# Kernel optimization log

Measured on AMD Instinct MI355X. Metric: run time of the kernel, lower is better.

Reference implementation:

```python
import jax, jax.numpy as jnp
import numpy as np

# DeepSeek-V2 MLA dims (one tensor-parallel shard of 8)
H = 5120          # hidden size
S = 2048          # seq len
B = 1
NH = 16           # 128 heads / 8 devices
Q_LORA = 1536
KV_LORA = 512
NOPE = 128
ROPE = 64
QK = NOPE + ROPE  # 192 per-head q/k dim
VD = 128          # v head dim
DEVICE_NUM = 8
EPS = 1e-6


def rms_norm(x, w):
    v = jnp.mean(jnp.square(x.astype(jnp.float32)), axis=-1, keepdims=True)
    return (x * jax.lax.rsqrt(v + EPS)).astype(x.dtype) * w


def rope_cos_sin(position_ids, dim=ROPE, base=10000.0):
    inv_freq = 1.0 / (base ** (jnp.arange(0, dim, 2, dtype=jnp.float32) / dim))
    freqs = position_ids.astype(jnp.float32)[..., None] * inv_freq       # [B,S,dim/2]
    emb = jnp.concatenate([freqs, freqs], axis=-1)                        # [B,S,dim]
    return jnp.cos(emb), jnp.sin(emb)


def apply_rope(x, cos, sin):
    # DeepSeek interleaved reorder: view(b,h,s,d//2,2).transpose(-1,-2).reshape
    b, h, s, d = x.shape
    x = x.reshape(b, h, s, d // 2, 2).transpose(0, 1, 2, 4, 3).reshape(b, h, s, d)
    x1, x2 = x[..., : d // 2], x[..., d // 2:]
    rot = jnp.concatenate([-x2, x1], axis=-1)
    return x * cos[:, None] + rot * sin[:, None]


def setup_inputs() -> dict:
    key = jax.random.key(0)
    ks = jax.random.split(key, 8)
    sc = 0.02
    hidden_states = jax.random.normal(ks[0], (B, S, H), dtype=jnp.float32)
    position_ids = jnp.arange(S, dtype=jnp.int64 if jax.config.jax_enable_x64 else jnp.int32)[None, :].repeat(B, 0)
    attention_mask = jnp.triu(jnp.full((S, S), -1e9, dtype=jnp.float32), 1)[None, None]
    return {
        "hidden_states": hidden_states,
        "position_ids": position_ids,
        "attention_mask": attention_mask,
        "ln_w": jnp.ones((H,), jnp.float32),
        "q_a_w": jax.random.normal(ks[1], (Q_LORA, H), jnp.float32) * sc,
        "q_a_ln_w": jnp.ones((Q_LORA,), jnp.float32),
        "q_b_w": jax.random.normal(ks[2], (NH * QK, Q_LORA), jnp.float32) * sc,
        "kv_a_w": jax.random.normal(ks[3], (KV_LORA + ROPE, H), jnp.float32) * sc,
        "kv_a_ln_w": jnp.ones((KV_LORA,), jnp.float32),
        "kv_b_w": jax.random.normal(ks[4], (NH * (NOPE + VD), KV_LORA), jnp.float32) * sc,
        "o_w": jax.random.normal(ks[5], (H, NH * VD), jnp.float32) * sc,
    }


def reference(hidden_states, position_ids, attention_mask, ln_w, q_a_w, q_a_ln_w,
              q_b_w, kv_a_w, kv_a_ln_w, kv_b_w, o_w):
    b, s, _ = hidden_states.shape
    residual = hidden_states * (1.0 / DEVICE_NUM)
    x = rms_norm(hidden_states, ln_w)

    # Q path: low-rank down-proj + RMSNorm + up-proj
    q = rms_norm(x @ q_a_w.T, q_a_ln_w) @ q_b_w.T                # [b,s,NH*QK]
    q = q.reshape(b, s, NH, QK).transpose(0, 2, 1, 3)            # [b,NH,s,QK]
    q_nope, q_pe = q[..., :NOPE], q[..., NOPE:]

    # KV path: compressed latent + shared rope key
    ckv = x @ kv_a_w.T                                           # [b,s,KV_LORA+ROPE]
    c_kv, k_pe = ckv[..., :KV_LORA], ckv[..., KV_LORA:]
    k_pe = k_pe.reshape(b, s, 1, ROPE).transpose(0, 2, 1, 3)     # [b,1,s,ROPE]
    kv = rms_norm(c_kv, kv_a_ln_w) @ kv_b_w.T                    # [b,s,NH*(NOPE+VD)]
    kv = kv.reshape(b, s, NH, NOPE + VD).transpose(0, 2, 1, 3)
    k_nope, v = kv[..., :NOPE], kv[..., NOPE:]

    cos, sin = rope_cos_sin(position_ids)
    q_pe = apply_rope(q_pe, cos, sin)
    k_pe = apply_rope(k_pe, cos, sin)

    k = jnp.concatenate([k_nope, jnp.broadcast_to(k_pe, (b, NH, s, ROPE))], axis=-1)
    qf = jnp.concatenate([q_nope, q_pe], axis=-1)

    scores = jnp.einsum('bhqd,bhkd->bhqk', qf, k) * (1.0 / np.sqrt(QK))
    scores = scores + attention_mask
    probs = jax.nn.softmax(scores, axis=-1)
    attn = jnp.einsum('bhqk,bhkd->bhqd', probs, v)               # [b,NH,s,VD]

    out = attn.transpose(0, 2, 1, 3).reshape(b, s, NH * VD) @ o_w.T
    hidden = residual + out
    return hidden.astype(jnp.float32), k.astype(jnp.float32), v.astype(jnp.float32)
```

## Files before the change

### kernel.cpp

```cpp
#include <hip/hip_runtime.h>
#include <math.h>

typedef unsigned short u16;
typedef unsigned int u32;
typedef __attribute__((ext_vector_type(8))) short short8;
typedef __attribute__((ext_vector_type(4))) float f32x4;

#define NHEADS 16
static const int S      = 2048;
static const int Hd     = 5120;
static const int QLORA  = 1536;
static const int KVLORA = 512;
static const int NQK    = 192;
static const int NVD    = 128;
static const int QDIM   = 3072;
static const int KVDIM  = 4096;
static const int NFUSE  = 2176;

__device__ __forceinline__ u16 f2bf(float f) {
    union { float f; u32 u; } v; v.f = f;
    u32 r = v.u + 0x7FFFu + ((v.u >> 16) & 1u);
    return (u16)(r >> 16);
}
__device__ __forceinline__ float bf2f(u16 h) {
    union { u32 u; float f; } v; v.u = (u32)h << 16; return v.f;
}

__global__ void convert_bf16_kernel(const float* __restrict__ src, u16* __restrict__ dst,
                                    int n_src, int n_total) {
    int i = (blockIdx.x * 256 + threadIdx.x) * 4;
    if (i >= n_total) return;
    union { u16 h[4]; uint2 u; } p;
    if (i < n_src) {
        float4 v = *(const float4*)(src + i);
        p.h[0] = f2bf(v.x); p.h[1] = f2bf(v.y); p.h[2] = f2bf(v.z); p.h[3] = f2bf(v.w);
    } else {
        p.h[0] = p.h[1] = p.h[2] = p.h[3] = 0;
    }
    *(uint2*)(dst + i) = p.u;
}

__global__ void rmsnorm_bf16_kernel(const float* in, const float* __restrict__ w,
                                    u16* out, int D, int in_stride, int out_stride) {
    int row = blockIdx.x;
    const float* x = in + (size_t)row * in_stride;
    u16* y = out + (size_t)row * out_stride;
    float ss = 0.f;
    for (int i = threadIdx.x; i < D; i += blockDim.x) { float v = x[i]; ss += v * v; }
    #pragma unroll
    for (int off = 32; off > 0; off >>= 1) ss += __shfl_xor(ss, off);
    __shared__ float wsum[8];
    int wid = threadIdx.x >> 6, lane = threadIdx.x & 63;
    if (lane == 0) wsum[wid] = ss;
    __syncthreads();
    float tot = 0.f;
    int nw = blockDim.x >> 6;
    for (int i = 0; i < nw; ++i) tot += wsum[i];
    float scale = rsqrtf(tot / (float)D + 1e-6f);
    for (int i = threadIdx.x; i < D; i += blockDim.x) y[i] = f2bf(x[i] * scale * w[i]);
}

__global__ void rmsnorm_bf16in_kernel(const u16* in, const float* __restrict__ w,
                                      u16* out, int D, int in_stride, int out_stride) {
    int row = blockIdx.x;
    const u16* x = in + (size_t)row * in_stride;
    u16* y = out + (size_t)row * out_stride;
    float ss = 0.f;
    for (int i = threadIdx.x; i < D; i += blockDim.x) { float v = bf2f(x[i]); ss += v * v; }
    #pragma unroll
    for (int off = 32; off > 0; off >>= 1) ss += __shfl_xor(ss, off);
    __shared__ float wsum[8];
    int wid = threadIdx.x >> 6, lane = threadIdx.x & 63;
    if (lane == 0) wsum[wid] = ss;
    __syncthreads();
    float tot = 0.f;
    int nw = blockDim.x >> 6;
    for (int i = 0; i < nw; ++i) tot += wsum[i];
    float scale = rsqrtf(tot / (float)D + 1e-6f);
    for (int i = threadIdx.x; i < D; i += blockDim.x) y[i] = f2bf(bf2f(x[i]) * scale * w[i]);
}

template<int BM, bool SWZ, bool OBF>
__global__ __launch_bounds__(256) void gemm_k(
    const u16* __restrict__ A, const u16* __restrict__ B, void* __restrict__ Cv,
    int M, int N, int K, const float* __restrict__ resid) {
    constexpr int MR = BM / 32;
    __shared__ u16 As[4][BM * 32];
    __shared__ u16 Bs[4][128 * 32];

    int bm, bn;
    if constexpr (SWZ) {
        const int lin = blockIdx.x + blockIdx.y * gridDim.x;
        const int nwg = gridDim.x * gridDim.y;
        const int xcd = lin & 7, off = lin >> 3;
        const int q = nwg >> 3, r = nwg & 7;
        const int wg = (xcd < r ? xcd * (q + 1) : r * (q + 1) + (xcd - r) * q) + off;
        bm = (wg % gridDim.y) * BM;
        bn = (wg / gridDim.y) * 128;
    } else {
        bm = blockIdx.y * BM;
        bn = blockIdx.x * 128;
    }

    const int tid = threadIdx.x;
    const int w = tid >> 6, lane = tid & 63;
    const int wr = w >> 1, wc = w & 1;
    const int fr = lane & 15, kg = lane >> 4;

    f32x4 acc[MR][4];
    #pragma unroll
    for (int i = 0; i < MR; ++i)
        #pragma unroll
        for (int j = 0; j < 4; ++j) acc[i][j] = (f32x4){0.f, 0.f, 0.f, 0.f};

    const int srow = lane >> 2;
    const int scol = (lane & 3) * 8;
    const u16* Ap0 = A + (size_t)(bm + w * (BM / 4) + srow) * K + scol;
    const u16* Ap1 = Ap0 + (size_t)16 * K;
    const u16* Bp0 = B + (size_t)(bn + w * 32 + srow) * K + scol;
    const u16* Bp1 = Bp0 + (size_t)16 * K;
    const int lda0 = (w * (BM / 4)) * 32;
    const int lda1 = (w * (BM / 4) + 16) * 32;
    const int ldb0 = (w * 32) * 32;
    const int ldb1 = (w * 32 + 16) * 32;

    auto STAGE = [&](int buf, int kk) {
        __builtin_amdgcn_global_load_lds(
            (const __attribute__((address_space(1))) void*)(Ap0 + kk),
            (__attribute__((address_space(3))) void*)&As[buf][lda0], 16, 0, 0);
        if constexpr (BM == 128)
            __builtin_amdgcn_global_load_lds(
                (const __attribute__((address_space(1))) void*)(Ap1 + kk),
                (__attribute__((address_space(3))) void*)&As[buf][lda1], 16, 0, 0);
        __builtin_amdgcn_global_load_lds(
            (const __attribute__((address_space(1))) void*)(Bp0 + kk),
            (__attribute__((address_space(3))) void*)&Bs[buf][ldb0], 16, 0, 0);
        __builtin_amdgcn_global_load_lds(
            (const __attribute__((address_space(1))) void*)(Bp1 + kk),
            (__attribute__((address_space(3))) void*)&Bs[buf][ldb1], 16, 0, 0);
    };
    auto COMP = [&](int buf) {
        short8 af[MR], bfr[4];
        #pragma unroll
        for (int i = 0; i < MR; ++i)
            af[i] = *(const short8*)&As[buf][(wr * (BM / 2) + i * 16 + fr) * 32 + kg * 8];
        #pragma unroll
        for (int i = 0; i < 4; ++i)
            bfr[i] = *(const short8*)&Bs[buf][(wc * 64 + i * 16 + fr) * 32 + kg * 8];
        #pragma unroll
        for (int mi = 0; mi < MR; ++mi)
            #pragma unroll
            for (int ni = 0; ni < 4; ++ni)
                acc[mi][ni] = __builtin_amdgcn_mfma_f32_16x16x32_bf16(af[mi], bfr[ni],
                                                                      acc[mi][ni], 0, 0, 0);
    };

    const int nk = K >> 5;
    STAGE(0, 0);
    STAGE(1, 32);
    for (int kt = 0; kt < nk; ++kt) {
        if (kt + 2 < nk) {
            STAGE((kt + 2) & 3, (kt + 2) << 5);
            if constexpr (BM == 128) asm volatile("s_waitcnt vmcnt(8)" ::: "memory");
            else                     asm volatile("s_waitcnt vmcnt(6)" ::: "memory");
        } else if (kt + 1 < nk) {
            if constexpr (BM == 128) asm volatile("s_waitcnt vmcnt(4)" ::: "memory");
            else                     asm volatile("s_waitcnt vmcnt(3)" ::: "memory");
        } else {
            asm volatile("s_waitcnt vmcnt(0)" ::: "memory");
        }
        __builtin_amdgcn_s_barrier();
        COMP(kt & 3);
    }

    #pragma unroll
    for (int mi = 0; mi < MR; ++mi)
        #pragma unroll
        for (int ni = 0; ni < 4; ++ni)
            #pragma unroll
            for (int r2 = 0; r2 < 4; ++r2) {
                int row = bm + wr * (BM / 2) + mi * 16 + kg * 4 + r2;
                int col = bn + wc * 64 + ni * 16 + fr;
                size_t idx = (size_t)row * N + col;
                float v = acc[mi][ni][r2];
                if constexpr (OBF) {
                    ((u16*)Cv)[idx] = f2bf(v);
                } else {
                    if (resid) v += resid[idx] * 0.125f;
                    ((float*)Cv)[idx] = v;
                }
            }
}

__global__ void prep_q_kernel(const u16* __restrict__ Qb, const int* __restrict__ pos,
                              u16* __restrict__ Qbf) {
    const int s = blockIdx.x;
    const int t = threadIdx.x;
    const u16* qrow = Qb + (size_t)s * QDIM;
    {
        int i = t * 4;
        int hh = i >> 7, d = i & 127;
        uint2 v = *(const uint2*)(qrow + hh * NQK + d);
        *(uint2*)(Qbf + ((size_t)hh * S + s) * NQK + d) = v;
    }
    {
        int hh = t >> 5, j = t & 31;
        float ps = (float)pos[s];
        float inv_freq = 1.0f / powf(10000.0f, (float)j * (1.0f / 32.0f));
        float ang = ps * inv_freq;
        float c = cosf(ang), sn = sinf(ang);
        const u16* pe = qrow + hh * NQK + 128;
        float a = bf2f(pe[2 * j]), b = bf2f(pe[2 * j + 1]);
        u16* dst = Qbf + ((size_t)hh * S + s) * NQK;
        dst[128 + j] = f2bf(a * c - b * sn);
        dst[160 + j] = f2bf(b * c + a * sn);
    }
}

__global__ __launch_bounds__(256) void build_kv64_kernel(
    const u16* __restrict__ KVb, const u16* __restrict__ CF,
    const int* __restrict__ pos_ids,
    float* __restrict__ Kout, float* __restrict__ Vout,
    u16* __restrict__ Kbf, u16* __restrict__ Vtb) {
    const int s0 = blockIdx.x * 64;
    const int h  = blockIdx.y;
    const int t  = threadIdx.x;
    __shared__ u16 T[64][132];

    #pragma unroll
    for (int it = 0; it < 4; ++it) {
        int i = t + it * 256;
        int row = i >> 4, c8 = (i & 15) * 8;
        int s = s0 + row;
        union { uint4 u; u16 hx[8]; } v;
        v.u = *(const uint4*)(KVb + (size_t)s * KVDIM + h * 256 + c8);
        size_t kidx = ((size_t)h * S + s) * NQK + c8;
        *(uint4*)(Kbf + kidx) = v.u;
        float4 f0 = {bf2f(v.hx[0]), bf2f(v.hx[1]), bf2f(v.hx[2]), bf2f(v.hx[3])};
        float4 f1 = {bf2f(v.hx[4]), bf2f(v.hx[5]), bf2f(v.hx[6]), bf2f(v.hx[7])};
        *(float4*)(Kout + kidx) = f0;
        *(float4*)(Kout + kidx + 4) = f1;
    }
    #pragma unroll
    for (int it = 0; it < 4; ++it) {
        int i = t + it * 256;
        int row = i >> 4, c8 = (i & 15) * 8;
        int s = s0 + row;
        union { uint4 u; uint2 d[2]; u16 hx[8]; } v;
        v.u = *(const uint4*)(KVb + (size_t)s * KVDIM + h * 256 + 128 + c8);
        *(uint2*)&T[row][c8]     = v.d[0];
        *(uint2*)&T[row][c8 + 4] = v.d[1];
        size_t vidx = ((size_t)h * S + s) * NVD + c8;
        float4 f0 = {bf2f(v.hx[0]), bf2f(v.hx[1]), bf2f(v.hx[2]), bf2f(v.hx[3])};
        float4 f1 = {bf2f(v.hx[4]), bf2f(v.hx[5]), bf2f(v.hx[6]), bf2f(v.hx[7])};
        *(float4*)(Vout + vidx) = f0;
        *(float4*)(Vout + vidx + 4) = f1;
    }
    #pragma unroll
    for (int it = 0; it < 8; ++it) {
        int i = t + it * 256;
        int row = i >> 5, j = i & 31;
        int s = s0 + row;
        float ps = (float)pos_ids[s];
        float inv_freq = 1.0f / powf(10000.0f, (float)j * (1.0f / 32.0f));
        float ang = ps * inv_freq;
        float c = cosf(ang), sn = sinf(ang);
        u32 pr = *(const u32*)(CF + (size_t)s * NFUSE + QLORA + KVLORA + 2 * j);
        float a = bf2f((u16)pr), b = bf2f((u16)(pr >> 16));
        float k0 = a * c - b * sn;
        float k1 = b * c + a * sn;
        size_t kidx = ((size_t)h * S + s) * NQK;
        Kout[kidx + 128 + j] = k0;
        Kout[kidx + 160 + j] = k1;
        Kbf[kidx + 128 + j] = f2bf(k0);
        Kbf[kidx + 160 + j] = f2bf(k1);
    }
    __syncthreads();
    const int d = t >> 1, half = t & 1;
    #pragma unroll
    for (int c = 0; c < 4; ++c) {
        u16 tmp[8];
        #pragma unroll
        for (int e = 0; e < 8; ++e) tmp[e] = T[half * 32 + c * 8 + e][d];
        *(uint4*)(Vtb + ((size_t)h * NVD + d) * S + s0 + half * 32 + c * 8) = *(uint4*)tmp;
    }
}

__global__ __launch_bounds__(256) void attn_mfma_kernel(
    const u16* __restrict__ Qbf, const u16* __restrict__ Kb,
    const u16* __restrict__ Vtb, u16* __restrict__ ATb) {
    const int h = blockIdx.y;
    const int q0 = blockIdx.x * 64;
    const int tid = threadIdx.x;
    const int w = tid >> 6, lane = tid & 63;
    const int fr = lane & 15, kg = lane >> 4;

    __shared__ __align__(16) u16 Ks[64 * 192];
    __shared__ __align__(16) u16 Vts[128 * 64];

    int kSrc[6], vSrc[4];
    #pragma unroll
    for (int i = 0; i < 6; ++i) {
        int D = (w * 6 + i) * 1024 + lane * 16;
        int row = D / 384, wb = D - row * 384;
        kSrc[i] = row * 384 + (wb ^ ((row & 7) << 4));
    }
    #pragma unroll
    for (int i = 0; i < 4; ++i) {
        int D = (w * 4 + i) * 1024 + lane * 16;
        int row = D >> 7, wb = D & 127;
        vSrc[i] = row * (S * 2) + (wb ^ ((row & 7) << 4));
    }
    const char* Kg = (const char*)(Kb + (size_t)h * S * NQK);
    const char* Vg = (const char*)(Vtb + (size_t)h * NVD * S);

    short8 qf[6];
    {
        const u16* qrow = Qbf + ((size_t)h * S + q0 + w * 16 + fr) * NQK;
        #pragma unroll
        for (int kb = 0; kb < 6; ++kb)
            qf[kb] = *(const short8*)(qrow + kb * 32 + kg * 8);
    }

    f32x4 o[8];
    #pragma unroll
    for (int ni = 0; ni < 8; ++ni) o[ni] = (f32x4){0.f, 0.f, 0.f, 0.f};
    float mrow = -1e30f, lrow = 0.f;
    const float scale = 0.0721687836487032f;
    const int qg = q0 + w * 16 + fr;
    const int swz = (fr & 7) << 4;

    for (int k0 = 0; k0 <= q0; k0 += 64) {
        __syncthreads();
        #pragma unroll
        for (int i = 0; i < 6; ++i)
            __builtin_amdgcn_global_load_lds(
                (const __attribute__((address_space(1))) void*)(Kg + (size_t)k0 * 384 + kSrc[i]),
                (__attribute__((address_space(3))) void*)((char*)Ks + (w * 6 + i) * 1024), 16, 0, 0);
        #pragma unroll
        for (int i = 0; i < 4; ++i)
            __builtin_amdgcn_global_load_lds(
                (const __attribute__((address_space(1))) void*)(Vg + (size_t)k0 * 2 + vSrc[i]),
                (__attribute__((address_space(3))) void*)((char*)Vts + (w * 4 + i) * 1024), 16, 0, 0);
        __syncthreads();

        f32x4 sacc[4];
        #pragma unroll
        for (int mi = 0; mi < 4; ++mi) sacc[mi] = (f32x4){0.f, 0.f, 0.f, 0.f};
        #pragma unroll
        for (int mi = 0; mi < 4; ++mi)
            #pragma unroll
            for (int kb = 0; kb < 6; ++kb) {
                const short8 kf = *(const short8*)((const char*)Ks +
                    (mi * 16 + fr) * 384 + ((kb * 64 + kg * 16) ^ swz));
                sacc[mi] = __builtin_amdgcn_mfma_f32_16x16x32_bf16(kf, qf[kb], sacc[mi], 0, 0, 0);
            }

        const bool diag = (k0 == q0);
        float p[4][4];
        float mx = -1e30f;
        #pragma unroll
        for (int mi = 0; mi < 4; ++mi)
            #pragma unroll
            for (int r = 0; r < 4; ++r) {
                float v = sacc[mi][r] * scale;
                if (diag && (k0 + mi * 16 + kg * 4 + r > qg)) v = -1e30f;
                p[mi][r] = v;
                mx = fmaxf(mx, v);
            }
        mx = fmaxf(mx, __shfl_xor(mx, 16));
        mx = fmaxf(mx, __shfl_xor(mx, 32));
        float mnew = fmaxf(mrow, mx);
        float corr = __expf(mrow - mnew);
        float psum = 0.f;
        #pragma unroll
        for (int mi = 0; mi < 4; ++mi)
            #pragma unroll
            for (int r = 0; r < 4; ++r) {
                float e = __expf(p[mi][r] - mnew);
                p[mi][r] = e;
                psum += e;
            }
        psum += __shfl_xor(psum, 16);
        psum += __shfl_xor(psum, 32);
        lrow = lrow * corr + psum;
        mrow = mnew;
        float corr_r[4];
        #pragma unroll
        for (int r = 0; r < 4; ++r) corr_r[r] = __shfl(corr, kg * 4 + r);
        #pragma unroll
        for (int ni = 0; ni < 8; ++ni) {
            o[ni][0] *= corr_r[0]; o[ni][1] *= corr_r[1];
            o[ni][2] *= corr_r[2]; o[ni][3] *= corr_r[3];
        }

        u32 pk0[4], pk1[4];
        #pragma unroll
        for (int mi = 0; mi < 4; ++mi) {
            pk0[mi] = (u32)f2bf(p[mi][0]) | ((u32)f2bf(p[mi][1]) << 16);
            pk1[mi] = (u32)f2bf(p[mi][2]) | ((u32)f2bf(p[mi][3]) << 16);
        }
        const int srcA = 2 * (kg & 1) * 16 + fr;
        const int srcB = srcA + 16;
        const int hsel = kg >> 1;
        short8 pa[2];
        #pragma unroll
        for (int ks = 0; ks < 2; ++ks) {
            u32 a0 = (u32)__shfl((int)pk0[ks * 2], srcA), b0 = (u32)__shfl((int)pk0[ks * 2 + 1], srcA);
            u32 a1 = (u32)__shfl((int)pk1[ks * 2], srcA), b1 = (u32)__shfl((int)pk1[ks * 2 + 1], srcA);
            u32 a2 = (u32)__shfl((int)pk0[ks * 2], srcB), b2 = (u32)__shfl((int)pk0[ks * 2 + 1], srcB);
            u32 a3 = (u32)__shfl((int)pk1[ks * 2], srcB), b3 = (u32)__shfl((int)pk1[ks * 2 + 1], srcB);
            union { u32 u[4]; short8 s8; } cvt;
            cvt.u[0] = hsel ? b0 : a0;
            cvt.u[1] = hsel ? b1 : a1;
            cvt.u[2] = hsel ? b2 : a2;
            cvt.u[3] = hsel ? b3 : a3;
            pa[ks] = cvt.s8;
        }

        #pragma unroll
        for (int ks = 0; ks < 2; ++ks)
            #pragma unroll
            for (int ni = 0; ni < 8; ++ni) {
                const short8 vf = *(const short8*)((const char*)Vts +
                    (ni * 16 + fr) * 128 + ((ks * 64 + kg * 16) ^ swz));
                o[ni] = __builtin_amdgcn_mfma_f32_16x16x32_bf16(pa[ks], vf, o[ni], 0, 0, 0);
            }
    }

    float inv = 1.f / lrow;
    float inv_r[4];
    #pragma unroll
    for (int r = 0; r < 4; ++r) inv_r[r] = __shfl(inv, kg * 4 + r);
    u16* outp = ATb + (size_t)(q0 + w * 16 + kg * 4) * (NHEADS * NVD) + h * NVD + fr;
    #pragma unroll
    for (int ni = 0; ni < 8; ++ni)
        #pragma unroll
        for (int r = 0; r < 4; ++r)
            outp[(size_t)r * (NHEADS * NVD) + ni * 16] = f2bf(o[ni][r] * inv_r[r]);
}

extern "C" void kernel_launch(void* const* d_in, const int* in_sizes, int n_in,
                              void* d_out, int out_size, void* d_ws, size_t ws_size,
                              hipStream_t stream) {
    (void)in_sizes; (void)n_in; (void)out_size; (void)ws_size;
    const float* hidden    = (const float*)d_in[0];
    const int*   pos       = (const int*)d_in[1];
    const float* ln_w      = (const float*)d_in[3];
    const float* q_a_w     = (const float*)d_in[4];
    const float* q_a_ln_w  = (const float*)d_in[5];
    const float* q_b_w     = (const float*)d_in[6];
    const float* kv_a_w    = (const float*)d_in[7];
    const float* kv_a_ln_w = (const float*)d_in[8];
    const float* kv_b_w    = (const float*)d_in[9];
    const float* o_w       = (const float*)d_in[10];

    float* OUT_H = (float*)d_out;
    float* OUT_K = OUT_H + (size_t)S * Hd;
    float* OUT_V = OUT_K + (size_t)NHEADS * S * NQK;

    char* ws = (char*)d_ws;
    u16*   o_wb    = (u16*)(ws);
    u16*   Wf      = (u16*)(ws + 20971520);
    u16*   Qbf     = (u16*)(ws + 20971520);
    u16*   Vtb     = (u16*)(ws + 33554432);
    u16*   Xb      = (u16*)(ws + 43253760);
    u16*   Kbf     = (u16*)(ws + 43253760);
    u16*   ATb     = (u16*)(ws + 55836672);
    u16*   CF      = (u16*)(ws + 64225280);
    u16*   QAn     = (u16*)(ws + 73138176);
    u16*   CKVN    = (u16*)(ws + 73138176);
    u16*   q_b_wb  = (u16*)(ws + 79429632);
    u16*   kv_b_wb = (u16*)(ws + 79429632);
    u16*   KVb     = (u16*)(ws + 88866816);
    u16*   Qb      = (u16*)(ws + 105644032);

    convert_bf16_kernel<<<(Hd * 2048 / 4 + 255) / 256, 256, 0, stream>>>(o_w, o_wb, Hd * 2048, Hd * 2048);
    convert_bf16_kernel<<<(QLORA * Hd / 4 + 255) / 256, 256, 0, stream>>>(q_a_w, Wf, QLORA * Hd, QLORA * Hd);
    convert_bf16_kernel<<<(640 * Hd / 4 + 255) / 256, 256, 0, stream>>>(kv_a_w, Wf + (size_t)QLORA * Hd, 576 * Hd, 640 * Hd);

    rmsnorm_bf16_kernel<<<S, 256, 0, stream>>>(hidden, ln_w, Xb, Hd, Hd, Hd);
    gemm_k<128, true, true><<<dim3(NFUSE / 128, S / 128), 256, 0, stream>>>(Xb, Wf, CF, S, NFUSE, Hd, nullptr);
    convert_bf16_kernel<<<(QDIM * QLORA / 4 + 255) / 256, 256, 0, stream>>>(q_b_w, q_b_wb, QDIM * QLORA, QDIM * QLORA);
    rmsnorm_bf16in_kernel<<<S, 256, 0, stream>>>(CF, q_a_ln_w, QAn, QLORA, NFUSE, QLORA);
    gemm_k<128, true, true><<<dim3(QDIM / 128, S / 128), 256, 0, stream>>>(QAn, q_b_wb, Qb, S, QDIM, QLORA, nullptr);
    convert_bf16_kernel<<<(KVDIM * KVLORA / 4 + 255) / 256, 256, 0, stream>>>(kv_b_w, kv_b_wb, KVDIM * KVLORA, KVDIM * KVLORA);
    rmsnorm_bf16in_kernel<<<S, 256, 0, stream>>>(CF + QLORA, kv_a_ln_w, CKVN, KVLORA, NFUSE, KVLORA);
    gemm_k<64, false, true><<<dim3(KVDIM / 128, S / 64), 256, 0, stream>>>(CKVN, kv_b_wb, KVb, S, KVDIM, KVLORA, nullptr);
    prep_q_kernel<<<S, 512, 0, stream>>>(Qb, pos, Qbf);
    build_kv64_kernel<<<dim3(S / 64, NHEADS), 256, 0, stream>>>(KVb, CF, pos, OUT_K, OUT_V, Kbf, Vtb);
    attn_mfma_kernel<<<dim3(S / 64, NHEADS), 256, 0, stream>>>(Qbf, Kbf, Vtb, ATb);
    gemm_k<64, false, false><<<dim3(Hd / 128, S / 64), 256, 0, stream>>>(ATb, o_wb, OUT_H, S, Hd, NHEADS * NVD, hidden);
}
```

Measured before the change: 420.2 us.

## Write Q head-major from GEMM epilogue, double-buffer attention K/V, reverse block order

```diff
diff --git a/kernel.cpp b/kernel.cpp
--- a/kernel.cpp
+++ b/kernel.cpp
@@ -80,7 +80,7 @@
     for (int i = threadIdx.x; i < D; i += blockDim.x) y[i] = f2bf(bf2f(x[i]) * scale * w[i]);
 }
 
-template<int BM, bool SWZ, bool OBF>
+template<int BM, bool SWZ, bool OBF, bool QPERM>
 __global__ __launch_bounds__(256) void gemm_k(
     const u16* __restrict__ A, const u16* __restrict__ B, void* __restrict__ Cv,
     int M, int N, int K, const float* __restrict__ resid) {
@@ -181,40 +181,33 @@
             for (int r2 = 0; r2 < 4; ++r2) {
                 int row = bm + wr * (BM / 2) + mi * 16 + kg * 4 + r2;
                 int col = bn + wc * 64 + ni * 16 + fr;
-                size_t idx = (size_t)row * N + col;
                 float v = acc[mi][ni][r2];
-                if constexpr (OBF) {
+                if constexpr (QPERM) {
+                    size_t idx = ((size_t)(col / 192) * S + row) * 192 + (col % 192);
                     ((u16*)Cv)[idx] = f2bf(v);
+                } else if constexpr (OBF) {
+                    ((u16*)Cv)[(size_t)row * N + col] = f2bf(v);
                 } else {
+                    size_t idx = (size_t)row * N + col;
                     if (resid) v += resid[idx] * 0.125f;
                     ((float*)Cv)[idx] = v;
                 }
             }
 }
 
-__global__ void prep_q_kernel(const u16* __restrict__ Qb, const int* __restrict__ pos,
-                              u16* __restrict__ Qbf) {
+__global__ void rope_q_inplace_kernel(u16* __restrict__ Qbf, const int* __restrict__ pos) {
     const int s = blockIdx.x;
     const int t = threadIdx.x;
-    const u16* qrow = Qb + (size_t)s * QDIM;
-    {
-        int i = t * 4;
-        int hh = i >> 7, d = i & 127;
-        uint2 v = *(const uint2*)(qrow + hh * NQK + d);
-        *(uint2*)(Qbf + ((size_t)hh * S + s) * NQK + d) = v;
-    }
-    {
-        int hh = t >> 5, j = t & 31;
-        float ps = (float)pos[s];
-        float inv_freq = 1.0f / powf(10000.0f, (float)j * (1.0f / 32.0f));
-        float ang = ps * inv_freq;
-        float c = cosf(ang), sn = sinf(ang);
-        const u16* pe = qrow + hh * NQK + 128;
-        float a = bf2f(pe[2 * j]), b = bf2f(pe[2 * j + 1]);
-        u16* dst = Qbf + ((size_t)hh * S + s) * NQK;
-        dst[128 + j] = f2bf(a * c - b * sn);
-        dst[160 + j] = f2bf(b * c + a * sn);
-    }
+    const int hh = t >> 5, j = t & 31;
+    float ps = (float)pos[s];
+    float inv_freq = 1.0f / powf(10000.0f, (float)j * (1.0f / 32.0f));
+    float ang = ps * inv_freq;
+    float c = cosf(ang), sn = sinf(ang);
+    u16* base = Qbf + ((size_t)hh * S + s) * NQK;
+    float a = bf2f(base[128 + 2 * j]), b = bf2f(base[128 + 2 * j + 1]);
+    __syncthreads();
+    base[128 + j] = f2bf(a * c - b * sn);
+    base[160 + j] = f2bf(b * c + a * sn);
 }
 
 __global__ __launch_bounds__(256) void build_kv64_kernel(
@@ -290,13 +283,13 @@
     const u16* __restrict__ Qbf, const u16* __restrict__ Kb,
     const u16* __restrict__ Vtb, u16* __restrict__ ATb) {
     const int h = blockIdx.y;
-    const int q0 = blockIdx.x * 64;
+    const int q0 = (gridDim.x - 1 - blockIdx.x) * 64;
     const int tid = threadIdx.x;
     const int w = tid >> 6, lane = tid & 63;
     const int fr = lane & 15, kg = lane >> 4;
 
-    __shared__ __align__(16) u16 Ks[64 * 192];
-    __shared__ __align__(16) u16 Vts[128 * 64];
+    __shared__ __align__(16) u16 Ks[2][64 * 192];
+    __shared__ __align__(16) u16 Vts[2][128 * 64];
 
     int kSrc[6], vSrc[4];
     #pragma unroll
@@ -313,6 +306,20 @@
     }
     const char* Kg = (const char*)(Kb + (size_t)h * S * NQK);
     const char* Vg = (const char*)(Vtb + (size_t)h * NVD * S);
+
+    auto STAGE = [&](int buf, int kt) {
+        const size_t krow = (size_t)kt * 64;
+        #pragma unroll
+        for (int i = 0; i < 6; ++i)
+            __builtin_amdgcn_global_load_lds(
+                (const __attribute__((address_space(1))) void*)(Kg + krow * 384 + kSrc[i]),
+                (__attribute__((address_space(3))) void*)((char*)&Ks[buf][0] + (w * 6 + i) * 1024), 16, 0, 0);
+        #pragma unroll
+        for (int i = 0; i < 4; ++i)
+            __builtin_amdgcn_global_load_lds(
+                (const __attribute__((address_space(1))) void*)(Vg + krow * 2 + vSrc[i]),
+                (__attribute__((address_space(3))) void*)((char*)&Vts[buf][0] + (w * 4 + i) * 1024), 16, 0, 0);
+    };
 
     short8 qf[6];
     {
@@ -329,32 +336,30 @@
     const float scale = 0.0721687836487032f;
     const int qg = q0 + w * 16 + fr;
     const int swz = (fr & 7) << 4;
-
-    for (int k0 = 0; k0 <= q0; k0 += 64) {
-        __syncthreads();
-        #pragma unroll
-        for (int i = 0; i < 6; ++i)
-            __builtin_amdgcn_global_load_lds(
-                (const __attribute__((address_space(1))) void*)(Kg + (size_t)k0 * 384 + kSrc[i]),
-                (__attribute__((address_space(3))) void*)((char*)Ks + (w * 6 + i) * 1024), 16, 0, 0);
-        #pragma unroll
-        for (int i = 0; i < 4; ++i)
-            __builtin_amdgcn_global_load_lds(
-                (const __attribute__((address_space(1))) void*)(Vg + (size_t)k0 * 2 + vSrc[i]),
-                (__attribute__((address_space(3))) void*)((char*)Vts + (w * 4 + i) * 1024), 16, 0, 0);
-        __syncthreads();
+    const int nt = (q0 >> 6) + 1;
+
+    STAGE(0, 0);
+    asm volatile("s_waitcnt vmcnt(0)" ::: "memory");
+    __builtin_amdgcn_s_barrier();
+
+    for (int t = 0; t < nt; ++t) {
+        if (t + 1 < nt) STAGE((t + 1) & 1, t + 1);
+        const int buf = t & 1;
+        const int k0 = t * 64;
 
         f32x4 sacc[4];
         #pragma unroll
         for (int mi = 0; mi < 4; ++mi) sacc[mi] = (f32x4){0.f, 0.f, 0.f, 0.f};
+        __builtin_amdgcn_s_setprio(1);
         #pragma unroll
         for (int mi = 0; mi < 4; ++mi)
             #pragma unroll
             for (int kb = 0; kb < 6; ++kb) {
-                const short8 kf = *(const short8*)((const char*)Ks +
+                const short8 kf = *(const short8*)((const char*)&Ks[buf][0] +
                     (mi * 16 + fr) * 384 + ((kb * 64 + kg * 16) ^ swz));
                 sacc[mi] = __builtin_amdgcn_mfma_f32_16x16x32_bf16(kf, qf[kb], sacc[mi], 0, 0, 0);
             }
+        __builtin_amdgcn_s_setprio(0);
 
         const bool diag = (k0 == q0);
         float p[4][4];
@@ -418,14 +423,19 @@
             pa[ks] = cvt.s8;
         }
 
+        __builtin_amdgcn_s_setprio(1);
         #pragma unroll
         for (int ks = 0; ks < 2; ++ks)
             #pragma unroll
             for (int ni = 0; ni < 8; ++ni) {
-                const short8 vf = *(const short8*)((const char*)Vts +
+                const short8 vf = *(const short8*)((const char*)&Vts[buf][0] +
                     (ni * 16 + fr) * 128 + ((ks * 64 + kg * 16) ^ swz));
                 o[ni] = __builtin_amdgcn_mfma_f32_16x16x32_bf16(pa[ks], vf, o[ni], 0, 0, 0);
             }
+        __builtin_amdgcn_s_setprio(0);
+
+        asm volatile("s_waitcnt vmcnt(0)" ::: "memory");
+        __builtin_amdgcn_s_barrier();
     }
 
     float inv = 1.f / lrow;
@@ -473,22 +483,21 @@
     u16*   q_b_wb  = (u16*)(ws + 79429632);
     u16*   kv_b_wb = (u16*)(ws + 79429632);
     u16*   KVb     = (u16*)(ws + 88866816);
-    u16*   Qb      = (u16*)(ws + 105644032);
 
     convert_bf16_kernel<<<(Hd * 2048 / 4 + 255) / 256, 256, 0, stream>>>(o_w, o_wb, Hd * 2048, Hd * 2048);
     convert_bf16_kernel<<<(QLORA * Hd / 4 + 255) / 256, 256, 0, stream>>>(q_a_w, Wf, QLORA * Hd, QLORA * Hd);
     convert_bf16_kernel<<<(640 * Hd / 4 + 255) / 256, 256, 0, stream>>>(kv_a_w, Wf + (size_t)QLORA * Hd, 576 * Hd, 640 * Hd);
 
     rmsnorm_bf16_kernel<<<S, 256, 0, stream>>>(hidden, ln_w, Xb, Hd, Hd, Hd);
-    gemm_k<128, true, true><<<dim3(NFUSE / 128, S / 128), 256, 0, stream>>>(Xb, Wf, CF, S, NFUSE, Hd, nullptr);
+    gemm_k<128, true, true, false><<<dim3(NFUSE / 128, S / 128), 256, 0, stream>>>(Xb, Wf, CF, S, NFUSE, Hd, nullptr);
     convert_bf16_kernel<<<(QDIM * QLORA / 4 + 255) / 256, 256, 0, stream>>>(q_b_w, q_b_wb, QDIM * QLORA, QDIM * QLORA);
     rmsnorm_bf16in_kernel<<<S, 256, 0, stream>>>(CF, q_a_ln_w, QAn, QLORA, NFUSE, QLORA);
-    gemm_k<128, true, true><<<dim3(QDIM / 128, S / 128), 256, 0, stream>>>(QAn, q_b_wb, Qb, S, QDIM, QLORA, nullptr);
+    gemm_k<128, true, true, true><<<dim3(QDIM / 128, S / 128), 256, 0, stream>>>(QAn, q_b_wb, Qbf, S, QDIM, QLORA, nullptr);
+    rope_q_inplace_kernel<<<S, 512, 0, stream>>>(Qbf, pos);
     convert_bf16_kernel<<<(KVDIM * KVLORA / 4 + 255) / 256, 256, 0, stream>>>(kv_b_w, kv_b_wb, KVDIM * KVLORA, KVDIM * KVLORA);
     rmsnorm_bf16in_kernel<<<S, 256, 0, stream>>>(CF + QLORA, kv_a_ln_w, CKVN, KVLORA, NFUSE, KVLORA);
-    gemm_k<64, false, true><<<dim3(KVDIM / 128, S / 64), 256, 0, stream>>>(CKVN, kv_b_wb, KVb, S, KVDIM, KVLORA, nullptr);
-    prep_q_kernel<<<S, 512, 0, stream>>>(Qb, pos, Qbf);
+    gemm_k<64, false, true, false><<<dim3(KVDIM / 128, S / 64), 256, 0, stream>>>(CKVN, kv_b_wb, KVb, S, KVDIM, KVLORA, nullptr);
     build_kv64_kernel<<<dim3(S / 64, NHEADS), 256, 0, stream>>>(KVb, CF, pos, OUT_K, OUT_V, Kbf, Vtb);
     attn_mfma_kernel<<<dim3(S / 64, NHEADS), 256, 0, stream>>>(Qbf, Kbf, Vtb, ATb);
-    gemm_k<64, false, false><<<dim3(Hd / 128, S / 64), 256, 0, stream>>>(ATb, o_wb, OUT_H, S, Hd, NHEADS * NVD, hidden);
-}
+    gemm_k<64, false, false, false><<<dim3(Hd / 128, S / 64), 256, 0, stream>>>(ATb, o_wb, OUT_H, S, Hd, NHEADS * NVD, hidden);
+}
```

Measured after the change: 418.5 us. No clear change (-0.4%).
